# Performance work log

Measured on AMD Instinct MI355X. Metric: run time of the kernel, lower is better.

## Reference

```python
import jax, jax.numpy as jnp
import numpy as np

N = 100000      # nodes
E = 3200000     # edges (before self loops)
IN = 128        # in_channels
H = 8           # heads
C = 16          # out_channels per head
NEG_SLOPE = 0.2


def setup_inputs() -> dict:
    key = jax.random.key(0)
    k1, k2, k3, k4, k5, k6 = jax.random.split(key, 6)
    x = jax.random.normal(k1, (N, IN), dtype=jnp.float32)
    edge_index = jax.random.randint(k2, (2, E), 0, N, dtype=jnp.int32)
    # GATConv params: lin weight [IN, H*C], att_src/att_dst [H, C], bias [H*C]
    W = jax.random.normal(k3, (IN, H * C), dtype=jnp.float32) / np.float32(np.sqrt(IN))
    att_src = jax.random.normal(k4, (H, C), dtype=jnp.float32) / np.float32(np.sqrt(C))
    att_dst = jax.random.normal(k5, (H, C), dtype=jnp.float32) / np.float32(np.sqrt(C))
    bias = jax.random.normal(k6, (H * C,), dtype=jnp.float32) * 0.01
    return {"x": x, "edge_index": edge_index, "W": W,
            "att_src": att_src, "att_dst": att_dst, "bias": bias}


def reference(x, edge_index, W, att_src, att_dst, bias):
    n = x.shape[0]
    h = (x @ W).reshape(n, H, C)                      # [N, H, C]
    # add self loops (PyG default add_self_loops=True)
    loop = jnp.arange(n, dtype=edge_index.dtype)
    src = jnp.concatenate([edge_index[0], loop])      # [E+N] message sources j
    dst = jnp.concatenate([edge_index[1], loop])      # [E+N] targets i
    # per-node attention logits
    a_src = jnp.einsum('nhc,hc->nh', h, att_src)      # [N, H]
    a_dst = jnp.einsum('nhc,hc->nh', h, att_dst)      # [N, H]
    alpha = jax.nn.leaky_relu(a_src[src] + a_dst[dst], NEG_SLOPE)  # [E+N, H]
    # segment softmax over edges grouped by destination node
    amax = jax.lax.stop_gradient(jax.ops.segment_max(alpha, dst, num_segments=n))
    ex = jnp.exp(alpha - amax[dst])
    denom = jax.ops.segment_sum(ex, dst, num_segments=n)           # [N, H]
    w = ex / (denom[dst] + 1e-16)                                  # [E+N, H]
    msg = h[src] * w[:, :, None]                                   # [E+N, H, C]
    out = jax.ops.segment_sum(msg, dst, num_segments=n)            # [N, H, C]
    return out.reshape(n, H * C) + bias
```

## Files before the change

### kernel.cpp

```cpp
#include <hip/hip_runtime.h>
#include <hip/hip_bf16.h>

#define H 8
#define C 16
#define HC 128
#define NEG 0.2f
#define XS_S 132

#define ANSH 6
#define AN 64
#define AMSK 63
#define CAP2 2560
#define MAXB2 2048
#define CB_SH 12
#define CBMSK 4095
#define MAXB1 64
#define EPB 4096

__device__ __forceinline__ float lrelu(float x) { return fmaxf(x, NEG * x); }

__device__ __forceinline__ unsigned pack_bf16(float a, float b) {
    union { __hip_bfloat16 h; unsigned short u; } ua, ub;
    ua.h = __float2bfloat16(a);
    ub.h = __float2bfloat16(b);
    return (unsigned)ua.u | ((unsigned)ub.u << 16);
}
__device__ __forceinline__ float bf_lo(unsigned d) { return __uint_as_float(d << 16); }
__device__ __forceinline__ float bf_hi(unsigned d) { return __uint_as_float(d & 0xffff0000u); }

__global__ void __launch_bounds__(256) k1_gemm(const float* __restrict__ x,
                                               const float* __restrict__ W,
                                               const float* __restrict__ att_src,
                                               const float* __restrict__ att_dst,
                                               unsigned* __restrict__ h16,
                                               float* __restrict__ a_src,
                                               float* __restrict__ a_dst, int N) {
    __shared__ float xs[64 * XS_S];
    const int n0 = blockIdx.x * 64;
    const int t = threadIdx.x;
#pragma unroll
    for (int i = 0; i < 8; ++i) {
        int id = t + 256 * i;
        int r = id >> 5, kq = id & 31;
        int n = n0 + r;
        float4 v = (n < N) ? ((const float4*)x)[(size_t)n * 32 + kq]
                           : make_float4(0.f, 0.f, 0.f, 0.f);
        *(float4*)&xs[r * XS_S + kq * 4] = v;
    }
    __syncthreads();
    const int cg = t & 31;
    const int r0 = (t >> 5) * 8;
    float acc[8][4];
#pragma unroll
    for (int i = 0; i < 8; ++i)
#pragma unroll
        for (int j = 0; j < 4; ++j) acc[i][j] = 0.f;

#pragma unroll 4
    for (int k = 0; k < HC; ++k) {
        const float4 wv = ((const float4*)W)[k * 32 + cg];
        float wr[4] = {wv.x, wv.y, wv.z, wv.w};
#pragma unroll
        for (int i = 0; i < 8; ++i) {
            float xv = xs[(r0 + i) * XS_S + k];
#pragma unroll
            for (int j = 0; j < 4; ++j) acc[i][j] += xv * wr[j];
        }
    }
    const int fhd = cg >> 2;
    const int cq  = cg & 3;
#pragma unroll
    for (int i = 0; i < 8; ++i) {
        int n = n0 + r0 + i;
        if (n < N) {
            uint2 dv = make_uint2(pack_bf16(acc[i][0], acc[i][1]),
                                  pack_bf16(acc[i][2], acc[i][3]));
            *(uint2*)&h16[(size_t)n * 64 + cg * 2] = dv;
        }
        float ps = 0.f, pd = 0.f;
#pragma unroll
        for (int jj = 0; jj < 4; ++jj) {
            float hv = acc[i][jj];
            ps += hv * att_src[fhd * C + cq * 4 + jj];
            pd += hv * att_dst[fhd * C + cq * 4 + jj];
        }
        ps += __shfl_xor(ps, 1, 4); pd += __shfl_xor(pd, 1, 4);
        ps += __shfl_xor(ps, 2, 4); pd += __shfl_xor(pd, 2, 4);
        if (cq == 0 && n < N) {
            a_src[(unsigned)n * 8u + fhd] = ps;
            a_dst[(unsigned)n * 8u + fhd] = pd;
        }
    }
}

__global__ void __launch_bounds__(256) kb_bin1(const int* __restrict__ ei,
                                               int* __restrict__ gcount1,
                                               unsigned* __restrict__ pairs1,
                                               int E, int NB1, int cap1) {
    __shared__ unsigned sp[EPB];
    __shared__ int hist[4][MAXB1];
    __shared__ int cur[4][MAXB1];
    __shared__ int tot[MAXB1];
    __shared__ int scn[MAXB1];
    __shared__ int gbase[MAXB1];
    const int t = threadIdx.x;
    const int wv = t >> 6;
    const int e0 = blockIdx.x * EPB;
    const int nE = min(EPB, E - e0);
    for (int i = t; i < 4 * MAXB1; i += 256) ((int*)hist)[i] = 0;
    __syncthreads();

    const bool v4 = ((E & 3) == 0) && ((nE & 3) == 0);
    const int nE4 = nE >> 2;
    const int4* d4p = (const int4*)(ei + E + e0);
    const int4* s4p = (const int4*)(ei + e0);
    if (v4) {
        for (int i = t; i < nE4; i += 256) {
            int4 d = d4p[i];
            atomicAdd(&hist[wv][d.x >> CB_SH], 1);
            atomicAdd(&hist[wv][d.y >> CB_SH], 1);
            atomicAdd(&hist[wv][d.z >> CB_SH], 1);
            atomicAdd(&hist[wv][d.w >> CB_SH], 1);
        }
    } else {
        for (int i = t; i < nE; i += 256)
            atomicAdd(&hist[wv][ei[E + e0 + i] >> CB_SH], 1);
    }
    __syncthreads();
    if (t < MAXB1) {
        int s = 0;
#pragma unroll
        for (int w = 0; w < 4; ++w) s += hist[w][t];
        tot[t] = s;
        scn[t] = s;
    }
    __syncthreads();
    for (int off = 1; off < MAXB1; off <<= 1) {
        int v = (t < MAXB1 && t >= off) ? scn[t - off] : 0;
        __syncthreads();
        if (t < MAXB1) scn[t] += v;
        __syncthreads();
    }
    if (t < MAXB1) {
        int h = tot[t];
        gbase[t] = h ? t * cap1 + atomicAdd(&gcount1[t], h) : 0;
        int off = scn[t] - h;
#pragma unroll
        for (int w = 0; w < 4; ++w) { cur[w][t] = off; off += hist[w][t]; }
    }
    __syncthreads();
    if (v4) {
        for (int i = t; i < nE4; i += 256) {
            int4 d = d4p[i];
            int4 sv = s4p[i];
#pragma unroll
            for (int q = 0; q < 4; ++q) {
                int dst = (&d.x)[q], src = (&sv.x)[q];
                int pos = atomicAdd(&cur[wv][dst >> CB_SH], 1);
                sp[pos] = (unsigned)src | ((unsigned)(dst & CBMSK) << 17);
            }
        }
    } else {
        for (int i = t; i < nE; i += 256) {
            int dst = ei[E + e0 + i], src = ei[e0 + i];
            int pos = atomicAdd(&cur[wv][dst >> CB_SH], 1);
            sp[pos] = (unsigned)src | ((unsigned)(dst & CBMSK) << 17);
        }
    }
    __syncthreads();
    const int lane = t & 63;
    for (int i = wv; i < NB1; i += 4) {
        int end = scn[i];
        int st  = (i > 0) ? scn[i - 1] : 0;
        int len = end - st;
        if (len <= 0) continue;
        int gb = gbase[i];
        int rem = i * cap1 + cap1 - gb;
        int wl = min(len, max(rem, 0));
        for (int k = lane; k < wl; k += 64)
            pairs1[gb + k] = sp[st + k];
    }
}

__global__ void __launch_bounds__(256) kb_bin2(const unsigned* __restrict__ pairs1,
                                               const int* __restrict__ gcount1,
                                               int* __restrict__ gcount2,
                                               unsigned* __restrict__ pairs2,
                                               int cap1, int ch2) {
    __shared__ unsigned sp[EPB];
    __shared__ int hist[4][64];
    __shared__ int cur[4][64];
    __shared__ int tot[64];
    __shared__ int scn[64];
    __shared__ int gbase[64];
    const int cb = blockIdx.x / ch2;
    const int ci = blockIdx.x % ch2;
    const int c1 = min(gcount1[cb], cap1);
    const int e0 = ci * EPB;
    if (e0 >= c1) return;
    const int nE = min(EPB, c1 - e0);
    const unsigned b1 = (unsigned)cb * (unsigned)cap1 + (unsigned)e0;
    const int t = threadIdx.x;
    const int wv = t >> 6;
    for (int i = t; i < 4 * 64; i += 256) ((int*)hist)[i] = 0;
    __syncthreads();

    const int nE4 = nE >> 2;
    const uint4* p4 = (const uint4*)(pairs1 + b1);
    for (int i = t; i < nE4; i += 256) {
        uint4 p = p4[i];
        atomicAdd(&hist[wv][p.x >> 23], 1);
        atomicAdd(&hist[wv][p.y >> 23], 1);
        atomicAdd(&hist[wv][p.z >> 23], 1);
        atomicAdd(&hist[wv][p.w >> 23], 1);
    }
    for (int i = (nE4 << 2) + t; i < nE; i += 256)
        atomicAdd(&hist[wv][pairs1[b1 + i] >> 23], 1);
    __syncthreads();
    if (t < 64) {
        int s = 0;
#pragma unroll
        for (int w = 0; w < 4; ++w) s += hist[w][t];
        tot[t] = s;
        scn[t] = s;
    }
    __syncthreads();
    for (int off = 1; off < 64; off <<= 1) {
        int v = (t < 64 && t >= off) ? scn[t - off] : 0;
        __syncthreads();
        if (t < 64) scn[t] += v;
        __syncthreads();
    }
    if (t < 64) {
        int h = tot[t];
        int gfb = cb * 64 + t;
        gbase[t] = h ? gfb * CAP2 + atomicAdd(&gcount2[gfb], h) : 0;
        int off = scn[t] - h;
#pragma unroll
        for (int w = 0; w < 4; ++w) { cur[w][t] = off; off += hist[w][t]; }
    }
    __syncthreads();
    for (int i = t; i < nE4; i += 256) {
        uint4 p = p4[i];
#pragma unroll
        for (int q = 0; q < 4; ++q) {
            unsigned pv = (&p.x)[q];
            int pos = atomicAdd(&cur[wv][pv >> 23], 1);
            sp[pos] = (pv & 0x1FFFFu) | (((pv >> 17) & 63u) << 18);
        }
    }
    for (int i = (nE4 << 2) + t; i < nE; i += 256) {
        unsigned pv = pairs1[b1 + i];
        int pos = atomicAdd(&cur[wv][pv >> 23], 1);
        sp[pos] = (pv & 0x1FFFFu) | (((pv >> 17) & 63u) << 18);
    }
    __syncthreads();
    const int lane = t & 63;
    for (int i = wv; i < 64; i += 4) {
        int end = scn[i];
        int st  = (i > 0) ? scn[i - 1] : 0;
        int len = end - st;
        if (len <= 0) continue;
        int gb = gbase[i];
        int fb0 = (cb * 64 + i) * CAP2;
        int rem = fb0 + CAP2 - gb;
        int wl = min(len, max(rem, 0));
        for (int k = lane; k < wl; k += 64)
            pairs2[gb + k] = sp[st + k];
    }
}

__global__ void __launch_bounds__(512) k_fused(const unsigned* __restrict__ pairs,
                                               const int* __restrict__ gcount,
                                               const unsigned* __restrict__ h16,
                                               const float* __restrict__ a_src,
                                               const float* __restrict__ a_dst,
                                               const float* __restrict__ bias,
                                               float* __restrict__ out, int N) {
    __shared__ int cnt[AN];
    __shared__ int sc[AN];
    __shared__ int lcur[AN];
    __shared__ int lbeg[AN + 1];
    __shared__ unsigned scol[CAP2];
    const int b = blockIdx.x;
    const int t = threadIdx.x;
    const int n0 = b << ANSH;
    const unsigned base = (unsigned)b * (unsigned)CAP2;
    const int cb = min(gcount[b], CAP2);

    if (t < AN) cnt[t] = 0;
    __syncthreads();
    for (int j = t; j < cb; j += 512)
        atomicAdd(&cnt[pairs[base + j] >> 18], 1);
    __syncthreads();
    if (t < AN) sc[t] = cnt[t];
    __syncthreads();
    for (int off = 1; off < AN; off <<= 1) {
        int v = (t < AN && t >= off) ? sc[t - off] : 0;
        __syncthreads();
        if (t < AN) sc[t] += v;
        __syncthreads();
    }
    if (t < AN) {
        lbeg[t + 1] = sc[t];
        lcur[t] = sc[t] - cnt[t];
        if (t == 0) lbeg[0] = 0;
    }
    __syncthreads();
    for (int j = t; j < cb; j += 512) {
        unsigned pv = pairs[base + j];
        int pos = atomicAdd(&lcur[pv >> 18], 1);
        scol[pos] = pv & 0x3FFFFu;
    }
    __syncthreads();

    const int wv = t >> 6;
    const int lane = t & 63;
    const int hd = lane >> 3;
    const int hw = lane & 7;
    const int bidx = hd * 4;

    for (int nl = wv; nl < AN; nl += 8) {
        const int node = n0 + nl;
        if (node >= N) break;
        const float adst_own = a_dst[(unsigned)node * 8u + (unsigned)hd];
        const float adst_hh  = a_dst[(unsigned)node * 8u + (unsigned)hw];
        const float wself = __expf(lrelu(a_src[(unsigned)node * 8u + (unsigned)hd] + adst_own));
        unsigned dself = h16[(unsigned)node * 64u + (unsigned)lane];
        float a0 = bf_lo(dself) * wself, a1 = bf_hi(dself) * wself;
        float b0 = 0.f, b1 = 0.f, c0 = 0.f, c1 = 0.f, e0 = 0.f, e1 = 0.f;
        float sA = wself, sB = 0.f, sC = 0.f, sD = 0.f;

        const int beg = lbeg[nl], end = lbeg[nl + 1];
        int j = beg;
        for (; j + 8 <= end; j += 8) {
            unsigned m0 = scol[j],     m1 = scol[j + 1], m2 = scol[j + 2], m3 = scol[j + 3];
            unsigned m4 = scol[j + 4], m5 = scol[j + 5], m6 = scol[j + 6], m7 = scol[j + 7];
            unsigned nP = scol[j + (lane >> 3)];
            float wme = __expf(lrelu(a_src[nP * 8u + (unsigned)hw] + adst_hh));
            int wi = __float_as_int(wme);
            float w0 = __int_as_float(__builtin_amdgcn_ds_bpermute(bidx,       wi));
            float w1 = __int_as_float(__builtin_amdgcn_ds_bpermute(bidx + 32,  wi));
            float w2 = __int_as_float(__builtin_amdgcn_ds_bpermute(bidx + 64,  wi));
            float w3 = __int_as_float(__builtin_amdgcn_ds_bpermute(bidx + 96,  wi));
            float w4 = __int_as_float(__builtin_amdgcn_ds_bpermute(bidx + 128, wi));
            float w5 = __int_as_float(__builtin_amdgcn_ds_bpermute(bidx + 160, wi));
            float w6 = __int_as_float(__builtin_amdgcn_ds_bpermute(bidx + 192, wi));
            float w7 = __int_as_float(__builtin_amdgcn_ds_bpermute(bidx + 224, wi));
            unsigned d0 = h16[m0 * 64u + (unsigned)lane];
            unsigned d1 = h16[m1 * 64u + (unsigned)lane];
            unsigned d2 = h16[m2 * 64u + (unsigned)lane];
            unsigned d3 = h16[m3 * 64u + (unsigned)lane];
            unsigned d4 = h16[m4 * 64u + (unsigned)lane];
            unsigned d5 = h16[m5 * 64u + (unsigned)lane];
            unsigned d6 = h16[m6 * 64u + (unsigned)lane];
            unsigned d7 = h16[m7 * 64u + (unsigned)lane];
            a0 += bf_lo(d0) * w0; a1 += bf_hi(d0) * w0; sA += w0;
            b0 += bf_lo(d1) * w1; b1 += bf_hi(d1) * w1; sB += w1;
            c0 += bf_lo(d2) * w2; c1 += bf_hi(d2) * w2; sC += w2;
            e0 += bf_lo(d3) * w3; e1 += bf_hi(d3) * w3; sD += w3;
            a0 += bf_lo(d4) * w4; a1 += bf_hi(d4) * w4; sA += w4;
            b0 += bf_lo(d5) * w5; b1 += bf_hi(d5) * w5; sB += w5;
            c0 += bf_lo(d6) * w6; c1 += bf_hi(d6) * w6; sC += w6;
            e0 += bf_lo(d7) * w7; e1 += bf_hi(d7) * w7; sD += w7;
        }
        if (j + 4 <= end) {
            unsigned m0 = scol[j], m1 = scol[j + 1], m2 = scol[j + 2], m3 = scol[j + 3];
            unsigned nP = scol[j + ((lane >> 3) & 3)];
            float wme = __expf(lrelu(a_src[nP * 8u + (unsigned)hw] + adst_hh));
            int wi = __float_as_int(wme);
            float w0 = __int_as_float(__builtin_amdgcn_ds_bpermute(bidx,      wi));
            float w1 = __int_as_float(__builtin_amdgcn_ds_bpermute(bidx + 32, wi));
            float w2 = __int_as_float(__builtin_amdgcn_ds_bpermute(bidx + 64, wi));
            float w3 = __int_as_float(__builtin_amdgcn_ds_bpermute(bidx + 96, wi));
            unsigned d0 = h16[m0 * 64u + (unsigned)lane];
            unsigned d1 = h16[m1 * 64u + (unsigned)lane];
            unsigned d2 = h16[m2 * 64u + (unsigned)lane];
            unsigned d3 = h16[m3 * 64u + (unsigned)lane];
            a0 += bf_lo(d0) * w0; a1 += bf_hi(d0) * w0; sA += w0;
            b0 += bf_lo(d1) * w1; b1 += bf_hi(d1) * w1; sB += w1;
            c0 += bf_lo(d2) * w2; c1 += bf_hi(d2) * w2; sC += w2;
            e0 += bf_lo(d3) * w3; e1 += bf_hi(d3) * w3; sD += w3;
            j += 4;
        }
        for (; j < end; ++j) {
            unsigned mA = scol[j];
            float wA = __expf(lrelu(a_src[mA * 8u + (unsigned)hd] + adst_own));
            unsigned dA = h16[mA * 64u + (unsigned)lane];
            a0 += bf_lo(dA) * wA; a1 += bf_hi(dA) * wA; sA += wA;
        }
        const float s = sA + sB + sC + sD;
        const float inv = 1.f / (s + 1e-16f);
        const float acc0 = a0 + b0 + c0 + e0;
        const float acc1 = a1 + b1 + c1 + e1;
        const float2 bv = ((const float2*)bias)[lane];
        float2 o;
        o.x = acc0 * inv + bv.x;
        o.y = acc1 * inv + bv.y;
        ((float2*)out)[(unsigned)node * 64u + (unsigned)lane] = o;
    }
}

extern "C" void kernel_launch(void* const* d_in, const int* in_sizes, int n_in,
                              void* d_out, int out_size, void* d_ws, size_t ws_size,
                              hipStream_t stream) {
    const float* x       = (const float*)d_in[0];
    const int*   ei      = (const int*)d_in[1];
    const float* W       = (const float*)d_in[2];
    const float* att_src = (const float*)d_in[3];
    const float* att_dst = (const float*)d_in[4];
    const float* bias    = (const float*)d_in[5];
    float* out = (float*)d_out;

    const int N = in_sizes[0] / HC;
    const int E = in_sizes[1] / 2;
    const int B = (N + AMSK) >> ANSH;
    const int NB1 = (N + CBMSK) >> CB_SH;
    const int nbin = (E + EPB - 1) / EPB;
    const int cap1 = (((E + NB1 - 1) / NB1) + 32768 + 3) & ~3;
    const int ch2 = (cap1 + EPB - 1) / EPB;

    unsigned* h16 = (unsigned*)d_ws;
    float* a_src  = (float*)(h16 + (size_t)N * 64);
    float* a_dst  = a_src + (size_t)N * H;
    int* gcount1  = (int*)(a_dst + (size_t)N * H);
    int* gcount2  = gcount1 + MAXB1;
    unsigned* pairs1 = (unsigned*)(gcount2 + MAXB2);
    unsigned* pairs2 = pairs1 + (size_t)NB1 * (size_t)cap1;

    static hipStream_t s_side = nullptr;
    static hipEvent_t ev_fork = nullptr, ev_join = nullptr;
    if (s_side == nullptr) {
        (void)hipStreamCreateWithFlags(&s_side, hipStreamNonBlocking);
        (void)hipEventCreateWithFlags(&ev_fork, hipEventDisableTiming);
        (void)hipEventCreateWithFlags(&ev_join, hipEventDisableTiming);
    }
    const bool fork = (s_side != nullptr && ev_fork != nullptr && ev_join != nullptr);
    hipStream_t sb = fork ? s_side : stream;

    if (fork) {
        (void)hipEventRecord(ev_fork, stream);
        (void)hipStreamWaitEvent(sb, ev_fork, 0);
    }

    (void)hipMemsetAsync(gcount1, 0, (MAXB1 + MAXB2) * sizeof(int), sb);
    kb_bin1<<<nbin, 256, 0, sb>>>(ei, gcount1, pairs1, E, NB1, cap1);
    kb_bin2<<<NB1 * ch2, 256, 0, sb>>>(pairs1, gcount1, gcount2, pairs2,
                                       cap1, ch2);
    if (fork) (void)hipEventRecord(ev_join, sb);

    k1_gemm<<<(N + 63) / 64, 256, 0, stream>>>(x, W, att_src, att_dst,
                                               h16, a_src, a_dst, N);

    if (fork) (void)hipStreamWaitEvent(stream, ev_join, 0);

    k_fused<<<B, 512, 0, stream>>>(pairs2, gcount2, h16, a_src,
                                   a_dst, bias, out, N);
}
```

Measured before the change: 375.6 us.

## Scatter binned edges directly to global, drop LDS staging and side stream

Both binning kernels now load their edge chunk into registers once. Each edge is then scattered straight to its global bucket position through per-wave atomic cursors seeded from the global base. This replaces the old path of staging into an LDS buffer, scanning, and copying out. The second kernel's prefix scan and the duplicate global reloads go away, and so does the side-stream fork/join that overlapped binning with the GEMM. The cost is uncoalesced global writes, and the binning now runs serially before the GEMM.

Result: faster. 353.9 us (-5.8%).

```diff
diff --git a/kernel.cpp b/kernel.cpp
--- a/kernel.cpp
+++ b/kernel.cpp
@@ -97,35 +97,51 @@
                                                int* __restrict__ gcount1,
                                                unsigned* __restrict__ pairs1,
                                                int E, int NB1, int cap1) {
-    __shared__ unsigned sp[EPB];
     __shared__ int hist[4][MAXB1];
     __shared__ int cur[4][MAXB1];
     __shared__ int tot[MAXB1];
     __shared__ int scn[MAXB1];
-    __shared__ int gbase[MAXB1];
     const int t = threadIdx.x;
     const int wv = t >> 6;
     const int e0 = blockIdx.x * EPB;
     const int nE = min(EPB, E - e0);
-    for (int i = t; i < 4 * MAXB1; i += 256) ((int*)hist)[i] = 0;
-    __syncthreads();
-
-    const bool v4 = ((E & 3) == 0) && ((nE & 3) == 0);
+    ((int*)hist)[t] = 0;
+    __syncthreads();
+
+    const bool al4 = ((E & 3) == 0);
     const int nE4 = nE >> 2;
+    int4 dreg[4], sreg[4];
     const int4* d4p = (const int4*)(ei + E + e0);
     const int4* s4p = (const int4*)(ei + e0);
-    if (v4) {
-        for (int i = t; i < nE4; i += 256) {
-            int4 d = d4p[i];
-            atomicAdd(&hist[wv][d.x >> CB_SH], 1);
-            atomicAdd(&hist[wv][d.y >> CB_SH], 1);
-            atomicAdd(&hist[wv][d.z >> CB_SH], 1);
-            atomicAdd(&hist[wv][d.w >> CB_SH], 1);
-        }
-    } else {
-        for (int i = t; i < nE; i += 256)
-            atomicAdd(&hist[wv][ei[E + e0 + i] >> CB_SH], 1);
-    }
+#pragma unroll
+    for (int j = 0; j < 4; ++j) {
+        int idx = j * 256 + t;
+        if (idx < nE4) {
+            if (al4) { dreg[j] = d4p[idx]; sreg[j] = s4p[idx]; }
+            else {
+                int e = idx * 4;
+                dreg[j] = make_int4(ei[E + e0 + e], ei[E + e0 + e + 1],
+                                    ei[E + e0 + e + 2], ei[E + e0 + e + 3]);
+                sreg[j] = make_int4(ei[e0 + e], ei[e0 + e + 1],
+                                    ei[e0 + e + 2], ei[e0 + e + 3]);
+            }
+        }
+    }
+    int tlD = 0, tlS = -1;
+    {
+        int tb = nE4 * 4 + t;
+        if (tb < nE) { tlD = ei[E + e0 + tb]; tlS = ei[e0 + tb]; }
+    }
+#pragma unroll
+    for (int j = 0; j < 4; ++j) {
+        if (j * 256 + t < nE4) {
+            atomicAdd(&hist[wv][dreg[j].x >> CB_SH], 1);
+            atomicAdd(&hist[wv][dreg[j].y >> CB_SH], 1);
+            atomicAdd(&hist[wv][dreg[j].z >> CB_SH], 1);
+            atomicAdd(&hist[wv][dreg[j].w >> CB_SH], 1);
+        }
+    }
+    if (tlS >= 0) atomicAdd(&hist[wv][tlD >> CB_SH], 1);
     __syncthreads();
     if (t < MAXB1) {
         int s = 0;
@@ -143,42 +159,29 @@
     }
     if (t < MAXB1) {
         int h = tot[t];
-        gbase[t] = h ? t * cap1 + atomicAdd(&gcount1[t], h) : 0;
-        int off = scn[t] - h;
-#pragma unroll
-        for (int w = 0; w < 4; ++w) { cur[w][t] = off; off += hist[w][t]; }
-    }
-    __syncthreads();
-    if (v4) {
-        for (int i = t; i < nE4; i += 256) {
-            int4 d = d4p[i];
-            int4 sv = s4p[i];
+        int gb = h ? t * cap1 + atomicAdd(&gcount1[t], h) : 0;
+#pragma unroll
+        for (int w = 0; w < 4; ++w) { cur[w][t] = gb; gb += hist[w][t]; }
+    }
+    __syncthreads();
+#pragma unroll
+    for (int j = 0; j < 4; ++j) {
+        if (j * 256 + t < nE4) {
 #pragma unroll
             for (int q = 0; q < 4; ++q) {
-                int dst = (&d.x)[q], src = (&sv.x)[q];
-                int pos = atomicAdd(&cur[wv][dst >> CB_SH], 1);
-                sp[pos] = (unsigned)src | ((unsigned)(dst & CBMSK) << 17);
+                int dst = (&dreg[j].x)[q], src = (&sreg[j].x)[q];
+                int b = dst >> CB_SH;
+                int pos = atomicAdd(&cur[wv][b], 1);
+                if (pos < b * cap1 + cap1)
+                    pairs1[pos] = (unsigned)src | ((unsigned)(dst & CBMSK) << 17);
             }
         }
-    } else {
-        for (int i = t; i < nE; i += 256) {
-            int dst = ei[E + e0 + i], src = ei[e0 + i];
-            int pos = atomicAdd(&cur[wv][dst >> CB_SH], 1);
-            sp[pos] = (unsigned)src | ((unsigned)(dst & CBMSK) << 17);
-        }
-    }
-    __syncthreads();
-    const int lane = t & 63;
-    for (int i = wv; i < NB1; i += 4) {
-        int end = scn[i];
-        int st  = (i > 0) ? scn[i - 1] : 0;
-        int len = end - st;
-        if (len <= 0) continue;
-        int gb = gbase[i];
-        int rem = i * cap1 + cap1 - gb;
-        int wl = min(len, max(rem, 0));
-        for (int k = lane; k < wl; k += 64)
-            pairs1[gb + k] = sp[st + k];
+    }
+    if (tlS >= 0) {
+        int b = tlD >> CB_SH;
+        int pos = atomicAdd(&cur[wv][b], 1);
+        if (pos < b * cap1 + cap1)
+            pairs1[pos] = (unsigned)tlS | ((unsigned)(tlD & CBMSK) << 17);
     }
 }
 
@@ -187,12 +190,9 @@
                                                int* __restrict__ gcount2,
                                                unsigned* __restrict__ pairs2,
                                                int cap1, int ch2) {
-    __shared__ unsigned sp[EPB];
     __shared__ int hist[4][64];
     __shared__ int cur[4][64];
     __shared__ int tot[64];
-    __shared__ int scn[64];
-    __shared__ int gbase[64];
     const int cb = blockIdx.x / ch2;
     const int ci = blockIdx.x % ch2;
     const int c1 = min(gcount1[cb], cap1);
@@ -202,71 +202,66 @@
     const unsigned b1 = (unsigned)cb * (unsigned)cap1 + (unsigned)e0;
     const int t = threadIdx.x;
     const int wv = t >> 6;
-    for (int i = t; i < 4 * 64; i += 256) ((int*)hist)[i] = 0;
+    ((int*)hist)[t] = 0;
     __syncthreads();
 
     const int nE4 = nE >> 2;
     const uint4* p4 = (const uint4*)(pairs1 + b1);
-    for (int i = t; i < nE4; i += 256) {
-        uint4 p = p4[i];
-        atomicAdd(&hist[wv][p.x >> 23], 1);
-        atomicAdd(&hist[wv][p.y >> 23], 1);
-        atomicAdd(&hist[wv][p.z >> 23], 1);
-        atomicAdd(&hist[wv][p.w >> 23], 1);
-    }
-    for (int i = (nE4 << 2) + t; i < nE; i += 256)
-        atomicAdd(&hist[wv][pairs1[b1 + i] >> 23], 1);
+    uint4 preg[4];
+#pragma unroll
+    for (int j = 0; j < 4; ++j) {
+        int idx = j * 256 + t;
+        if (idx < nE4) preg[j] = p4[idx];
+    }
+    unsigned tlP = 0; int tlV = 0;
+    {
+        int tb = nE4 * 4 + t;
+        if (tb < nE) { tlP = pairs1[b1 + tb]; tlV = 1; }
+    }
+#pragma unroll
+    for (int j = 0; j < 4; ++j) {
+        if (j * 256 + t < nE4) {
+            atomicAdd(&hist[wv][preg[j].x >> 23], 1);
+            atomicAdd(&hist[wv][preg[j].y >> 23], 1);
+            atomicAdd(&hist[wv][preg[j].z >> 23], 1);
+            atomicAdd(&hist[wv][preg[j].w >> 23], 1);
+        }
+    }
+    if (tlV) atomicAdd(&hist[wv][tlP >> 23], 1);
     __syncthreads();
     if (t < 64) {
         int s = 0;
 #pragma unroll
         for (int w = 0; w < 4; ++w) s += hist[w][t];
         tot[t] = s;
-        scn[t] = s;
-    }
-    __syncthreads();
-    for (int off = 1; off < 64; off <<= 1) {
-        int v = (t < 64 && t >= off) ? scn[t - off] : 0;
-        __syncthreads();
-        if (t < 64) scn[t] += v;
-        __syncthreads();
-    }
+    }
+    __syncthreads();
     if (t < 64) {
         int h = tot[t];
         int gfb = cb * 64 + t;
-        gbase[t] = h ? gfb * CAP2 + atomicAdd(&gcount2[gfb], h) : 0;
-        int off = scn[t] - h;
-#pragma unroll
-        for (int w = 0; w < 4; ++w) { cur[w][t] = off; off += hist[w][t]; }
-    }
-    __syncthreads();
-    for (int i = t; i < nE4; i += 256) {
-        uint4 p = p4[i];
-#pragma unroll
-        for (int q = 0; q < 4; ++q) {
-            unsigned pv = (&p.x)[q];
-            int pos = atomicAdd(&cur[wv][pv >> 23], 1);
-            sp[pos] = (pv & 0x1FFFFu) | (((pv >> 17) & 63u) << 18);
-        }
-    }
-    for (int i = (nE4 << 2) + t; i < nE; i += 256) {
-        unsigned pv = pairs1[b1 + i];
-        int pos = atomicAdd(&cur[wv][pv >> 23], 1);
-        sp[pos] = (pv & 0x1FFFFu) | (((pv >> 17) & 63u) << 18);
-    }
-    __syncthreads();
-    const int lane = t & 63;
-    for (int i = wv; i < 64; i += 4) {
-        int end = scn[i];
-        int st  = (i > 0) ? scn[i - 1] : 0;
-        int len = end - st;
-        if (len <= 0) continue;
-        int gb = gbase[i];
-        int fb0 = (cb * 64 + i) * CAP2;
-        int rem = fb0 + CAP2 - gb;
-        int wl = min(len, max(rem, 0));
-        for (int k = lane; k < wl; k += 64)
-            pairs2[gb + k] = sp[st + k];
+        int gb = h ? gfb * CAP2 + atomicAdd(&gcount2[gfb], h) : 0;
+#pragma unroll
+        for (int w = 0; w < 4; ++w) { cur[w][t] = gb; gb += hist[w][t]; }
+    }
+    __syncthreads();
+#pragma unroll
+    for (int j = 0; j < 4; ++j) {
+        if (j * 256 + t < nE4) {
+#pragma unroll
+            for (int q = 0; q < 4; ++q) {
+                unsigned pv = (&preg[j].x)[q];
+                int fb = pv >> 23;
+                int pos = atomicAdd(&cur[wv][fb], 1);
+                if (pos < (cb * 64 + fb) * CAP2 + CAP2)
+                    pairs2[pos] = (pv & 0x1FFFFu) | (((pv >> 17) & 63u) << 18);
+            }
+        }
+    }
+    if (tlV) {
+        int fb = tlP >> 23;
+        int pos = atomicAdd(&cur[wv][fb], 1);
+        if (pos < (cb * 64 + fb) * CAP2 + CAP2)
+            pairs2[pos] = (tlP & 0x1FFFFu) | (((tlP >> 17) & 63u) << 18);
     }
 }
 
@@ -428,32 +423,12 @@
     unsigned* pairs1 = (unsigned*)(gcount2 + MAXB2);
     unsigned* pairs2 = pairs1 + (size_t)NB1 * (size_t)cap1;
 
-    static hipStream_t s_side = nullptr;
-    static hipEvent_t ev_fork = nullptr, ev_join = nullptr;
-    if (s_side == nullptr) {
-        (void)hipStreamCreateWithFlags(&s_side, hipStreamNonBlocking);
-        (void)hipEventCreateWithFlags(&ev_fork, hipEventDisableTiming);
-        (void)hipEventCreateWithFlags(&ev_join, hipEventDisableTiming);
-    }
-    const bool fork = (s_side != nullptr && ev_fork != nullptr && ev_join != nullptr);
-    hipStream_t sb = fork ? s_side : stream;
-
-    if (fork) {
-        (void)hipEventRecord(ev_fork, stream);
-        (void)hipStreamWaitEvent(sb, ev_fork, 0);
-    }
-
-    (void)hipMemsetAsync(gcount1, 0, (MAXB1 + MAXB2) * sizeof(int), sb);
-    kb_bin1<<<nbin, 256, 0, sb>>>(ei, gcount1, pairs1, E, NB1, cap1);
-    kb_bin2<<<NB1 * ch2, 256, 0, sb>>>(pairs1, gcount1, gcount2, pairs2,
-                                       cap1, ch2);
-    if (fork) (void)hipEventRecord(ev_join, sb);
-
+    (void)hipMemsetAsync(gcount1, 0, (MAXB1 + MAXB2) * sizeof(int), stream);
+    kb_bin1<<<nbin, 256, 0, stream>>>(ei, gcount1, pairs1, E, NB1, cap1);
+    kb_bin2<<<NB1 * ch2, 256, 0, stream>>>(pairs1, gcount1, gcount2, pairs2,
+                                           cap1, ch2);
     k1_gemm<<<(N + 63) / 64, 256, 0, stream>>>(x, W, att_src, att_dst,
                                                h16, a_src, a_dst, N);
-
-    if (fork) (void)hipStreamWaitEvent(stream, ev_join, 0);
-
     k_fused<<<B, 512, 0, stream>>>(pairs2, gcount2, h16, a_src,
                                    a_dst, bias, out, N);
 }
```
